# Optimization experiments

Hardware: AMD Instinct MI355X
Metric: run time of the kernel (lower is better)

The kernel has to match this reference:

```python
import jax, jax.numpy as jnp
import numpy as np

N_SRC, N_DST, E, D = 100000, 100000, 1250000, 64


def setup_inputs() -> dict:
    key = jax.random.key(0)
    k1, k2, k3, k4 = jax.random.split(key, 4)
    h_src = jax.random.normal(k1, (N_SRC, D), dtype=jnp.float32)
    mask = jax.random.uniform(k2, (E,), dtype=jnp.float32)
    src_idx = jax.random.randint(k3, (E,), 0, N_SRC, dtype=jnp.int32)
    dst_idx = jax.random.randint(k4, (E,), 0, N_DST, dtype=jnp.int32)
    return {"h_src": h_src, "mask": mask, "src_idx": src_idx,
            "dst_idx": dst_idx, "n_dst": N_DST}


def reference(h_src, mask, src_idx, dst_idx, n_dst):
    # h_src: [N_src, D]; mask: [E]; src_idx/dst_idx: [E]
    n_src = h_src.shape[0]
    ones = jnp.ones(src_idx.shape[0], dtype=h_src.dtype)
    # out-degree normalization of source features (deg^-0.5, clamped at 1)
    out_deg = jnp.clip(jax.ops.segment_sum(ones, src_idx, num_segments=n_src), 1.0, None)
    feat_src = h_src * (out_deg ** -0.5)[:, None]
    # message = src feature * edge mask; reduce = segment-sum at destination
    msgs = feat_src[src_idx] * mask[:, None]            # [E, D]
    rst = jax.ops.segment_sum(msgs, dst_idx, num_segments=n_dst)  # [N_dst, D]
    # in-degree normalization of result
    in_deg = jnp.clip(jax.ops.segment_sum(ones, dst_idx, num_segments=n_dst), 1.0, None)
    return rst * (in_deg ** -0.5)[:, None]
```

## Files before the change

kernel.cpp:

```cpp
#include <hip/hip_runtime.h>
#include <hip/hip_fp16.h>

#define D 64
#define TILE_W 64
#define LOG_TW 6
#define MAXT 1600
#define NB 256
#define CAPE 1024
#define BIG 1024

__device__ inline void block_exscan_1024(const int* __restrict__ hist,
                                         int* __restrict__ loc,
                                         int n, int* __restrict__ sc) {
    int tid = threadIdx.x;
    int i0 = 2 * tid, i1 = i0 + 1;
    int v0 = (i0 < n) ? hist[i0] : 0;
    int v1 = (i1 < n) ? hist[i1] : 0;
    sc[tid] = v0 + v1;
    __syncthreads();
    for (int off = 1; off < 1024; off <<= 1) {
        int x = (tid >= off) ? sc[tid - off] : 0;
        __syncthreads();
        sc[tid] += x;
        __syncthreads();
    }
    int excl = sc[tid] - (v0 + v1);
    if (i0 < n) loc[i0] = excl;
    if (i1 < n) loc[i1] = excl + v0;
    if (tid == 0) loc[n] = sc[1023];
    __syncthreads();
}

__global__ __launch_bounds__(1024) void p3_sortplace(
        const float* __restrict__ mask,
        const int* __restrict__ src_idx,
        const int* __restrict__ dst_idx,
        int E, int Td, int Ts, int C,
        int2* __restrict__ csrD,
        unsigned char* __restrict__ srcb,
        int* __restrict__ locD,
        int* __restrict__ locS) {
    __shared__ int histD[MAXT];
    __shared__ int histS[MAXT];
    __shared__ int curD[MAXT + 1];
    __shared__ int curS[MAXT + 1];
    __shared__ int sc[1024];
    int b = blockIdx.x;
    int lo = b * C, hi = min(E, lo + C);
    for (int t = threadIdx.x; t < Td; t += 1024) histD[t] = 0;
    for (int t = threadIdx.x; t < Ts; t += 1024) histS[t] = 0;
    __syncthreads();
    for (int e = lo + threadIdx.x; e < hi; e += 1024) {
        atomicAdd(&histD[dst_idx[e] >> LOG_TW], 1);
        atomicAdd(&histS[src_idx[e] >> LOG_TW], 1);
    }
    __syncthreads();
    block_exscan_1024(histD, curD, Td, sc);
    block_exscan_1024(histS, curS, Ts, sc);
    for (int t = threadIdx.x; t <= Td; t += 1024) locD[(size_t)b * (Td + 1) + t] = curD[t];
    for (int t = threadIdx.x; t <= Ts; t += 1024) locS[(size_t)b * (Ts + 1) + t] = curS[t];
    __syncthreads();
    for (int e = lo + threadIdx.x; e < hi; e += 1024) {
        int s = src_idx[e], d = dst_idx[e];
        int pd = atomicAdd(&curD[d >> LOG_TW], 1);
        csrD[lo + pd] = make_int2((s << LOG_TW) | (d & (TILE_W - 1)),
                                  __float_as_int(mask[e]));
        int ps = atomicAdd(&curS[s >> LOG_TW], 1);
        srcb[lo + ps] = (unsigned char)(s & (TILE_W - 1));
    }
}

__global__ void p3b_rdeg(const unsigned char* __restrict__ srcb,
                         const int* __restrict__ locS,
                         int Ts, int C, int n_src,
                         float* __restrict__ rdeg) {
    __shared__ int hist[TILE_W];
    int t = blockIdx.x;
    if (threadIdx.x < TILE_W) hist[threadIdx.x] = 0;
    __syncthreads();
    for (int b = threadIdx.x; b < NB; b += blockDim.x) {
        int base = b * C;
        int s0 = locS[(size_t)b * (Ts + 1) + t];
        int s1 = locS[(size_t)b * (Ts + 1) + t + 1];
        for (int i = base + s0; i < base + s1; ++i)
            atomicAdd(&hist[srcb[i]], 1);
    }
    __syncthreads();
    if (threadIdx.x < TILE_W) {
        int g = t * TILE_W + threadIdx.x;
        if (g < n_src) rdeg[g] = rsqrtf((float)max(hist[threadIdx.x], 1));
    }
}

__global__ void p3c_feat(const float* __restrict__ h_src,
                         const float* __restrict__ rdeg,
                         int n_src,
                         uint2* __restrict__ feat) {
    int N = n_src * (D / 4);
    int i = blockIdx.x * blockDim.x + threadIdx.x;
    int stride = gridDim.x * blockDim.x;
    for (; i < N; i += stride) {
        float4 v = ((const float4*)h_src)[i];
        float rs = rdeg[i >> 4];
        __half2 lo = __halves2half2(__float2half(v.x * rs), __float2half(v.y * rs));
        __half2 hi = __halves2half2(__float2half(v.z * rs), __float2half(v.w * rs));
        union { __half2 h2[2]; uint2 u; } pk;
        pk.h2[0] = lo; pk.h2[1] = hi;
        feat[i] = pk.u;
    }
}

__global__ __launch_bounds__(512) void p4_gather(
        const __half2* __restrict__ feat,
        const int2* __restrict__ csrD,
        const int* __restrict__ locD,
        int Td, int C, int n_dst,
        float* __restrict__ out) {
    __shared__ int2 ebuf[CAPE];
    __shared__ int2 ebuf2[CAPE];
    __shared__ int hist[TILE_W];
    __shared__ int dstart[TILE_W];
    __shared__ int cur[TILE_W];
    __shared__ int natom;
    int t = blockIdx.x;
    int tid = threadIdx.x;
    for (int i = tid; i < TILE_W; i += blockDim.x) hist[i] = 0;
    if (tid == 0) natom = 0;
    __syncthreads();

    for (int b = tid; b < NB; b += blockDim.x) {
        int base = b * C;
        int s0 = locD[(size_t)b * (Td + 1) + t];
        int s1 = locD[(size_t)b * (Td + 1) + t + 1];
        int len = s1 - s0;
        if (len <= 0) continue;
        int pos = atomicAdd(&natom, len);
        for (int i = 0; i < len; ++i) {
            if (pos + i < CAPE) {
                int2 ent = csrD[base + s0 + i];
                ebuf[pos + i] = ent;
                atomicAdd(&hist[ent.x & (TILE_W - 1)], 1);
            }
        }
    }
    __syncthreads();
    int n_e = min(natom, CAPE);

    if (tid < 64) {
        int v = hist[tid];
        int incl = v;
        for (int off = 1; off < 64; off <<= 1) {
            int u = __shfl_up(incl, off, 64);
            if (tid >= off) incl += u;
        }
        dstart[tid] = incl - v;
        cur[tid]    = incl - v;
    }
    __syncthreads();

    for (int i = tid; i < n_e; i += blockDim.x) {
        int2 ent = ebuf[i];
        int pos = atomicAdd(&cur[ent.x & (TILE_W - 1)], 1);
        ebuf2[pos] = make_int2(ent.x >> LOG_TW, ent.y);
    }
    __syncthreads();

    int wid = tid >> 6, lane = tid & 63;
    int h = lane >> 5, s = lane & 31;
    int nw = blockDim.x >> 6;
    int dpw = TILE_W / nw;
    for (int k = 0; k < dpw; ++k) {
        int d = wid * dpw + k;
        int dg = t * TILE_W + d;
        if (dg >= n_dst) continue;
        int n = hist[d], st = dstart[d];
        float a0x = 0.f, a0y = 0.f, a1x = 0.f, a1y = 0.f;
        int j = 0;
        for (; j + 4 <= n; j += 4) {
            int2 eA = ebuf2[st + j + h];
            int2 eB = ebuf2[st + j + 2 + h];
            __half2 fA = feat[(size_t)eA.x * 32 + s];
            __half2 fB = feat[(size_t)eB.x * 32 + s];
            float cA = __int_as_float(eA.y);
            float cB = __int_as_float(eB.y);
            a0x += cA * __low2float(fA);  a0y += cA * __high2float(fA);
            a1x += cB * __low2float(fB);  a1y += cB * __high2float(fB);
        }
        for (; j < n; j += 2) {
            bool val = (j + h) < n;
            int2 e = ebuf2[val ? (st + j + h) : st];
            float c = val ? __int_as_float(e.y) : 0.f;
            __half2 f = feat[(size_t)e.x * 32 + s];
            a0x += c * __low2float(f);  a0y += c * __high2float(f);
        }
        float ax = a0x + a1x, ay = a0y + a1y;
        ax += __shfl_xor(ax, 32, 64);
        ay += __shfl_xor(ay, 32, 64);
        if (h == 0) {
            float rn = rsqrtf((float)max(n, 1));
            ((float2*)out)[(size_t)dg * 32 + s] = make_float2(ax * rn, ay * rn);
        }
    }
}

__global__ void fill_kernel(const float* __restrict__ mask,
                            const int* __restrict__ src_idx,
                            const int* __restrict__ dst_idx,
                            int E,
                            int* __restrict__ out_deg,
                            int* __restrict__ cursor,
                            int2* __restrict__ sorted) {
    int i = blockIdx.x * blockDim.x + threadIdx.x;
    int stride = gridDim.x * blockDim.x;
    for (int e = i; e < E; e += stride) {
        int s = src_idx[e];
        int t = dst_idx[e];
        atomicAdd(&out_deg[s], 1);
        int pos = atomicAdd(&cursor[t], 1);
        if (pos < 64) {
            int2 m; m.x = s; m.y = __float_as_int(mask[e]);
            sorted[(size_t)t * 64 + pos] = m;
        }
    }
}

__global__ void gatherF_kernel(const float* __restrict__ h_src,
                               const int* __restrict__ out_deg,
                               const int* __restrict__ cursor,
                               const int2* __restrict__ sorted,
                               int n_dst,
                               float* __restrict__ out) {
    int wid  = threadIdx.x >> 6;
    int lane = threadIdx.x & 63;
    int t = blockIdx.x * (blockDim.x >> 6) + wid;
    if (t >= n_dst) return;
    int n = min(cursor[t], 64);
    int   s_mine = 0;
    float c_mine = 0.f;
    if (lane < n) {
        int2 m = sorted[(size_t)t * 64 + lane];
        s_mine = m.x;
        c_mine = __int_as_float(m.y) * rsqrtf((float)max(out_deg[m.x], 1));
    }
    float acc = 0.f;
    for (int j = 0; j < n; ++j) {
        int   s = __shfl(s_mine, j, 64);
        float c = __shfl(c_mine, j, 64);
        acc += c * h_src[(size_t)s * D + lane];
    }
    out[(size_t)t * D + lane] = acc * rsqrtf((float)max(n, 1));
}

extern "C" void kernel_launch(void* const* d_in, const int* in_sizes, int n_in,
                              void* d_out, int out_size, void* d_ws, size_t ws_size,
                              hipStream_t stream) {
    const float* h_src   = (const float*)d_in[0];
    const float* mask    = (const float*)d_in[1];
    const int*   src_idx = (const int*)d_in[2];
    const int*   dst_idx = (const int*)d_in[3];
    int n_src = in_sizes[0] / D;
    int E     = in_sizes[1];
    int n_dst = out_size / D;
    float* out = (float*)d_out;

    int Td = (n_dst + TILE_W - 1) / TILE_W;
    int Ts = (n_src + TILE_W - 1) / TILE_W;
    int C  = (E + NB - 1) / NB;

    auto al = [](size_t x) { return (x + 255) & ~(size_t)255; };
    size_t off_csr  = 0;
    size_t off_srcb = al(off_csr + (size_t)E * sizeof(int2));
    size_t off_locD = al(off_srcb + (size_t)E);
    size_t off_locS = al(off_locD + (size_t)NB * (Td + 1) * sizeof(int));
    size_t off_rdeg = al(off_locS + (size_t)NB * (Ts + 1) * sizeof(int));
    size_t off_feat = al(off_rdeg + (size_t)n_src * sizeof(float));
    size_t need     = off_feat + (size_t)n_src * D * sizeof(__half);

    if (ws_size >= need && Td <= MAXT && Ts <= MAXT &&
        n_src <= (1 << 25) && (D % 4) == 0) {
        int2*          csrD = (int2*)((char*)d_ws + off_csr);
        unsigned char* srcb = (unsigned char*)((char*)d_ws + off_srcb);
        int*           locD = (int*)((char*)d_ws + off_locD);
        int*           locS = (int*)((char*)d_ws + off_locS);
        float*         rdeg = (float*)((char*)d_ws + off_rdeg);
        uint2*         feat = (uint2*)((char*)d_ws + off_feat);

        p3_sortplace<<<NB, BIG, 0, stream>>>(mask, src_idx, dst_idx,
                                             E, Td, Ts, C, csrD, srcb, locD, locS);
        p3b_rdeg<<<Ts, 256, 0, stream>>>(srcb, locS, Ts, C, n_src, rdeg);
        p3c_feat<<<2048, 256, 0, stream>>>(h_src, rdeg, n_src, feat);
        p4_gather<<<Td, 512, 0, stream>>>((const __half2*)feat, csrD, locD,
                                          Td, C, n_dst, out);
    } else {
        int*  out_deg = (int*)d_ws;
        int*  cursor  = out_deg + n_src;
        int2* sorted  = (int2*)(cursor + n_dst);
        hipMemsetAsync(d_ws, 0, (size_t)(n_src + n_dst) * sizeof(int), stream);
        fill_kernel<<<2048, 256, 0, stream>>>(mask, src_idx, dst_idx, E,
                                              out_deg, cursor, sorted);
        int blocks = (n_dst + 3) / 4;
        gatherF_kernel<<<blocks, 256, 0, stream>>>(h_src, out_deg, cursor, sorted,
                                                   n_dst, out);
    }
}
```

Baseline: 89.16 us.

## Fuse degree and feature-scale kernels; restructure gather staging and widen lane loads

Merges the out-degree histogram kernel with the fp16 feature scaling kernel, so each source tile computes its rsqrt degrees in shared memory and scales its own rows, removing one launch and the rdeg buffer. In the gather kernel, the intermediate shared edge buffer is dropped: segment bounds are loaded in parallel and two threads per bucket read csrD twice (histogram pass, then placement pass) instead of serial per-thread copying. The per-destination accumulation now uses 16 lanes with 8-byte loads, covering four edges per wave step, and reduces across lane quarters with shuffles. The trade-off is a second global read of csrD and extra shuffle reductions.

```diff
diff --git a/kernel.cpp b/kernel.cpp
--- a/kernel.cpp
+++ b/kernel.cpp
@@ -70,15 +70,18 @@
     }
 }
 
-__global__ void p3b_rdeg(const unsigned char* __restrict__ srcb,
-                         const int* __restrict__ locS,
-                         int Ts, int C, int n_src,
-                         float* __restrict__ rdeg) {
+__global__ void p3bc_feat(const unsigned char* __restrict__ srcb,
+                          const int* __restrict__ locS,
+                          const float* __restrict__ h_src,
+                          int Ts, int C, int n_src,
+                          uint2* __restrict__ feat) {
     __shared__ int hist[TILE_W];
+    __shared__ float rs[TILE_W];
     int t = blockIdx.x;
-    if (threadIdx.x < TILE_W) hist[threadIdx.x] = 0;
-    __syncthreads();
-    for (int b = threadIdx.x; b < NB; b += blockDim.x) {
+    int tid = threadIdx.x;
+    if (tid < TILE_W) hist[tid] = 0;
+    __syncthreads();
+    for (int b = tid; b < NB; b += blockDim.x) {
         int base = b * C;
         int s0 = locS[(size_t)b * (Ts + 1) + t];
         int s1 = locS[(size_t)b * (Ts + 1) + t + 1];
@@ -86,65 +89,51 @@
             atomicAdd(&hist[srcb[i]], 1);
     }
     __syncthreads();
-    if (threadIdx.x < TILE_W) {
-        int g = t * TILE_W + threadIdx.x;
-        if (g < n_src) rdeg[g] = rsqrtf((float)max(hist[threadIdx.x], 1));
-    }
-}
-
-__global__ void p3c_feat(const float* __restrict__ h_src,
-                         const float* __restrict__ rdeg,
-                         int n_src,
-                         uint2* __restrict__ feat) {
-    int N = n_src * (D / 4);
-    int i = blockIdx.x * blockDim.x + threadIdx.x;
-    int stride = gridDim.x * blockDim.x;
-    for (; i < N; i += stride) {
-        float4 v = ((const float4*)h_src)[i];
-        float rs = rdeg[i >> 4];
-        __half2 lo = __halves2half2(__float2half(v.x * rs), __float2half(v.y * rs));
-        __half2 hi = __halves2half2(__float2half(v.z * rs), __float2half(v.w * rs));
+    if (tid < TILE_W) rs[tid] = rsqrtf((float)max(hist[tid], 1));
+    __syncthreads();
+    int base_row = t * TILE_W;
+    int nrows = min(TILE_W, n_src - base_row);
+    int total = nrows * 16;
+    for (int i = tid; i < total; i += blockDim.x) {
+        int r = i >> 4, sub = i & 15;
+        float4 v = ((const float4*)h_src)[(size_t)(base_row + r) * 16 + sub];
+        float sc2 = rs[r];
+        __half2 lo2 = __halves2half2(__float2half(v.x * sc2), __float2half(v.y * sc2));
+        __half2 hi2 = __halves2half2(__float2half(v.z * sc2), __float2half(v.w * sc2));
         union { __half2 h2[2]; uint2 u; } pk;
-        pk.h2[0] = lo; pk.h2[1] = hi;
-        feat[i] = pk.u;
+        pk.h2[0] = lo2; pk.h2[1] = hi2;
+        feat[(size_t)(base_row + r) * 16 + sub] = pk.u;
     }
 }
 
 __global__ __launch_bounds__(512) void p4_gather(
-        const __half2* __restrict__ feat,
+        const uint2* __restrict__ feat,
         const int2* __restrict__ csrD,
         const int* __restrict__ locD,
         int Td, int C, int n_dst,
         float* __restrict__ out) {
-    __shared__ int2 ebuf[CAPE];
     __shared__ int2 ebuf2[CAPE];
+    __shared__ int2 segs[NB];
     __shared__ int hist[TILE_W];
     __shared__ int dstart[TILE_W];
     __shared__ int cur[TILE_W];
-    __shared__ int natom;
     int t = blockIdx.x;
     int tid = threadIdx.x;
-    for (int i = tid; i < TILE_W; i += blockDim.x) hist[i] = 0;
-    if (tid == 0) natom = 0;
-    __syncthreads();
-
-    for (int b = tid; b < NB; b += blockDim.x) {
-        int base = b * C;
-        int s0 = locD[(size_t)b * (Td + 1) + t];
-        int s1 = locD[(size_t)b * (Td + 1) + t + 1];
-        int len = s1 - s0;
-        if (len <= 0) continue;
-        int pos = atomicAdd(&natom, len);
-        for (int i = 0; i < len; ++i) {
-            if (pos + i < CAPE) {
-                int2 ent = csrD[base + s0 + i];
-                ebuf[pos + i] = ent;
-                atomicAdd(&hist[ent.x & (TILE_W - 1)], 1);
-            }
-        }
-    }
-    __syncthreads();
-    int n_e = min(natom, CAPE);
+    if (tid < TILE_W) hist[tid] = 0;
+    if (tid < NB) {
+        int s0 = locD[(size_t)tid * (Td + 1) + t];
+        int s1 = locD[(size_t)tid * (Td + 1) + t + 1];
+        segs[tid] = make_int2(tid * C + s0, tid * C + s1);
+    }
+    __syncthreads();
+
+    {
+        int b = tid >> 1;
+        int2 sg = segs[b];
+        for (int i = sg.x + (tid & 1); i < sg.y; i += 2)
+            atomicAdd(&hist[csrD[i].x & (TILE_W - 1)], 1);
+    }
+    __syncthreads();
 
     if (tid < 64) {
         int v = hist[tid];
@@ -158,47 +147,63 @@
     }
     __syncthreads();
 
-    for (int i = tid; i < n_e; i += blockDim.x) {
-        int2 ent = ebuf[i];
-        int pos = atomicAdd(&cur[ent.x & (TILE_W - 1)], 1);
-        ebuf2[pos] = make_int2(ent.x >> LOG_TW, ent.y);
+    {
+        int b = tid >> 1;
+        int2 sg = segs[b];
+        for (int i = sg.x + (tid & 1); i < sg.y; i += 2) {
+            int2 ent = csrD[i];
+            int pos = atomicAdd(&cur[ent.x & (TILE_W - 1)], 1);
+            ebuf2[min(pos, CAPE - 1)] = make_int2(ent.x >> LOG_TW, ent.y);
+        }
     }
     __syncthreads();
 
     int wid = tid >> 6, lane = tid & 63;
-    int h = lane >> 5, s = lane & 31;
-    int nw = blockDim.x >> 6;
-    int dpw = TILE_W / nw;
-    for (int k = 0; k < dpw; ++k) {
-        int d = wid * dpw + k;
+    int q = lane >> 4, sub = lane & 15;
+    for (int k = 0; k < TILE_W / 8; ++k) {
+        int d = wid * 8 + k;
         int dg = t * TILE_W + d;
         if (dg >= n_dst) continue;
         int n = hist[d], st = dstart[d];
-        float a0x = 0.f, a0y = 0.f, a1x = 0.f, a1y = 0.f;
-        int j = 0;
-        for (; j + 4 <= n; j += 4) {
-            int2 eA = ebuf2[st + j + h];
-            int2 eB = ebuf2[st + j + 2 + h];
-            __half2 fA = feat[(size_t)eA.x * 32 + s];
-            __half2 fB = feat[(size_t)eB.x * 32 + s];
-            float cA = __int_as_float(eA.y);
-            float cB = __int_as_float(eB.y);
-            a0x += cA * __low2float(fA);  a0y += cA * __high2float(fA);
-            a1x += cB * __low2float(fB);  a1y += cB * __high2float(fB);
-        }
-        for (; j < n; j += 2) {
-            bool val = (j + h) < n;
-            int2 e = ebuf2[val ? (st + j + h) : st];
-            float c = val ? __int_as_float(e.y) : 0.f;
-            __half2 f = feat[(size_t)e.x * 32 + s];
-            a0x += c * __low2float(f);  a0y += c * __high2float(f);
-        }
-        float ax = a0x + a1x, ay = a0y + a1y;
-        ax += __shfl_xor(ax, 32, 64);
-        ay += __shfl_xor(ay, 32, 64);
-        if (h == 0) {
+        float4 a0 = make_float4(0.f, 0.f, 0.f, 0.f);
+        float4 a1 = make_float4(0.f, 0.f, 0.f, 0.f);
+        for (int j = 0; j < n; j += 8) {
+            {
+                bool val = (j + q) < n;
+                int idx = val ? min(st + j + q, CAPE - 1) : 0;
+                int2 e = ebuf2[idx];
+                float c = val ? __int_as_float(e.y) : 0.f;
+                int row = val ? e.x : 0;
+                uint2 f = feat[(size_t)row * 16 + sub];
+                union { uint2 u; __half2 h2[2]; } pk; pk.u = f;
+                float2 f0 = __half22float2(pk.h2[0]);
+                float2 f1 = __half22float2(pk.h2[1]);
+                a0.x += c * f0.x; a0.y += c * f0.y;
+                a0.z += c * f1.x; a0.w += c * f1.y;
+            }
+            {
+                bool val = (j + 4 + q) < n;
+                int idx = val ? min(st + j + 4 + q, CAPE - 1) : 0;
+                int2 e = ebuf2[idx];
+                float c = val ? __int_as_float(e.y) : 0.f;
+                int row = val ? e.x : 0;
+                uint2 f = feat[(size_t)row * 16 + sub];
+                union { uint2 u; __half2 h2[2]; } pk; pk.u = f;
+                float2 f0 = __half22float2(pk.h2[0]);
+                float2 f1 = __half22float2(pk.h2[1]);
+                a1.x += c * f0.x; a1.y += c * f0.y;
+                a1.z += c * f1.x; a1.w += c * f1.y;
+            }
+        }
+        float4 acc = make_float4(a0.x + a1.x, a0.y + a1.y, a0.z + a1.z, a0.w + a1.w);
+        acc.x += __shfl_xor(acc.x, 16, 64); acc.x += __shfl_xor(acc.x, 32, 64);
+        acc.y += __shfl_xor(acc.y, 16, 64); acc.y += __shfl_xor(acc.y, 32, 64);
+        acc.z += __shfl_xor(acc.z, 16, 64); acc.z += __shfl_xor(acc.z, 32, 64);
+        acc.w += __shfl_xor(acc.w, 16, 64); acc.w += __shfl_xor(acc.w, 32, 64);
+        if (q == 0) {
             float rn = rsqrtf((float)max(n, 1));
-            ((float2*)out)[(size_t)dg * 32 + s] = make_float2(ax * rn, ay * rn);
+            ((float4*)out)[(size_t)dg * 16 + sub] =
+                make_float4(acc.x * rn, acc.y * rn, acc.z * rn, acc.w * rn);
         }
     }
 }
@@ -272,8 +277,7 @@
     size_t off_srcb = al(off_csr + (size_t)E * sizeof(int2));
     size_t off_locD = al(off_srcb + (size_t)E);
     size_t off_locS = al(off_locD + (size_t)NB * (Td + 1) * sizeof(int));
-    size_t off_rdeg = al(off_locS + (size_t)NB * (Ts + 1) * sizeof(int));
-    size_t off_feat = al(off_rdeg + (size_t)n_src * sizeof(float));
+    size_t off_feat = al(off_locS + (size_t)NB * (Ts + 1) * sizeof(int));
     size_t need     = off_feat + (size_t)n_src * D * sizeof(__half);
 
     if (ws_size >= need && Td <= MAXT && Ts <= MAXT &&
@@ -282,15 +286,12 @@
         unsigned char* srcb = (unsigned char*)((char*)d_ws + off_srcb);
         int*           locD = (int*)((char*)d_ws + off_locD);
         int*           locS = (int*)((char*)d_ws + off_locS);
-        float*         rdeg = (float*)((char*)d_ws + off_rdeg);
         uint2*         feat = (uint2*)((char*)d_ws + off_feat);
 
         p3_sortplace<<<NB, BIG, 0, stream>>>(mask, src_idx, dst_idx,
                                              E, Td, Ts, C, csrD, srcb, locD, locS);
-        p3b_rdeg<<<Ts, 256, 0, stream>>>(srcb, locS, Ts, C, n_src, rdeg);
-        p3c_feat<<<2048, 256, 0, stream>>>(h_src, rdeg, n_src, feat);
-        p4_gather<<<Td, 512, 0, stream>>>((const __half2*)feat, csrD, locD,
-                                          Td, C, n_dst, out);
+        p3bc_feat<<<Ts, 256, 0, stream>>>(srcb, locS, h_src, Ts, C, n_src, feat);
+        p4_gather<<<Td, 512, 0, stream>>>(feat, csrD, locD, Td, C, n_dst, out);
     } else {
         int*  out_deg = (int*)d_ws;
         int*  cursor  = out_deg + n_src;
```

Result: faster. 82.63 us (-7.3%).
